# Kernel tuning notes

Hardware: AMD Instinct MI355X
Metric: run time of the kernel (lower is better)

## Reference

```python
import jax, jax.numpy as jnp
import numpy as np

EPS = 1e-13

def masked_softmax(scores, mask):
    # scores: [B, L1, L2], mask: [B, L2] binary float
    # ESIM-style: softmax(scores * mask) * mask, renormalized.
    m = mask[:, None, :]                      # [B, 1, L2]
    r = jax.nn.softmax(scores * m, axis=-1) * m
    return r / (r.sum(axis=-1, keepdims=True) + EPS)

def weighted_sum(attn, tensor, mask):
    # attn: [B, L1, L2], tensor: [B, L2, D], mask: [B, L1]
    return jnp.matmul(attn, tensor) * mask[:, :, None]

def setup_inputs() -> dict:
    key = jax.random.key(0)
    k1, k2, k3, k4 = jax.random.split(key, 4)
    B, Lp, Lh, D = 64, 512, 512, 600
    encoded_premise = jax.random.normal(k1, (B, Lp, D), dtype=jnp.float32)
    encoded_hypothesis = jax.random.normal(k2, (B, Lh, D), dtype=jnp.float32)
    # binary padding masks (1 = valid token)
    premise_mask = (jax.random.uniform(k3, (B, Lp)) > 0.15).astype(jnp.float32)
    hypothesis_mask = (jax.random.uniform(k4, (B, Lh)) > 0.15).astype(jnp.float32)
    return {"encoded_premise": encoded_premise, "premise_mask": premise_mask,
            "encoded_hypothesis": encoded_hypothesis, "hypothesis_mask": hypothesis_mask}

def reference(encoded_premise, premise_mask, encoded_hypothesis, hypothesis_mask):
    # shared cross-attention score matrix [B, Lp, Lh]
    attn = jnp.einsum('bpd,bhd->bph', encoded_premise, encoded_hypothesis)
    a_p = masked_softmax(attn, hypothesis_mask)                    # [B, Lp, Lh]
    a_h = masked_softmax(attn.transpose(0, 2, 1), premise_mask)    # [B, Lh, Lp]
    weighted_premise = weighted_sum(a_p, encoded_hypothesis, premise_mask)      # [B, Lp, D]
    weighted_hypothesis = weighted_sum(a_h, encoded_premise, hypothesis_mask)   # [B, Lh, D]
    return (weighted_premise, weighted_hypothesis)
```

## Files before the change

### kernel.cpp

```cpp
#include <hip/hip_runtime.h>
#include <hip/hip_bf16.h>

#define DEVB 64
#define LSEQ 512
#define DDIM 600
#define KPAD 608

typedef short short8 __attribute__((ext_vector_type(8)));
typedef float f32x4 __attribute__((ext_vector_type(4)));
typedef _Float16 f16x8 __attribute__((ext_vector_type(8)));
typedef _Float16 f16x4 __attribute__((ext_vector_type(4)));

constexpr int LDP = 40;

__device__ __forceinline__ unsigned short f2bf(float x) {
    union { float f; unsigned u; } v; v.f = x;
    unsigned r = v.u + 0x7fffu + ((v.u >> 16) & 1u);
    return (unsigned short)(r >> 16);
}
__device__ __forceinline__ f32x4 mfma16(short8 a, short8 b, f32x4 c) {
    return __builtin_amdgcn_mfma_f32_16x16x32_bf16(a, b, c, 0, 0, 0);
}
__device__ __forceinline__ f32x4 mfma16h(f16x8 a, f16x8 b, f32x4 c) {
    return __builtin_amdgcn_mfma_f32_16x16x32_f16(a, b, c, 0, 0, 0);
}

__global__ __launch_bounds__(256) void prep(
    const float* __restrict__ X, _Float16* __restrict__ Xhi,
    _Float16* __restrict__ Xlo)
{
    int g = blockIdx.x * 256 + threadIdx.x;
    int row  = g / 152;
    int slot = g - row * 152;
    int d = slot << 2;
    f16x4 hi = {0, 0, 0, 0}, lo = {0, 0, 0, 0};
    if (d < DDIM) {
        float4 x = *(const float4*)(X + (size_t)row * DDIM + d);
        hi[0] = (_Float16)x.x; lo[0] = (_Float16)(x.x - (float)hi[0]);
        hi[1] = (_Float16)x.y; lo[1] = (_Float16)(x.y - (float)hi[1]);
        hi[2] = (_Float16)x.z; lo[2] = (_Float16)(x.z - (float)hi[2]);
        hi[3] = (_Float16)x.w; lo[3] = (_Float16)(x.w - (float)hi[3]);
    }
    *(f16x4*)(Xhi + (size_t)row * KPAD + d) = hi;
    if (Xlo) *(f16x4*)(Xlo + (size_t)row * KPAD + d) = lo;
}

__global__ __launch_bounds__(256) void attn_gemm(
    const _Float16* __restrict__ Phi, const _Float16* __restrict__ Plo,
    const _Float16* __restrict__ Hhi, float* __restrict__ attn)
{
    const int bid = blockIdx.x;
    const int swz = (bid & 7) * 128 + (bid >> 3);
    const int b  = swz >> 4;
    const int pt = ((swz >> 2) & 3) << 7;
    const int ht = (swz & 3) << 7;
    const _Float16* Pbh = Phi + (size_t)b * LSEQ * KPAD;
    const _Float16* Pbl = Plo + (size_t)b * LSEQ * KPAD;
    const _Float16* Hb  = Hhi + (size_t)b * LSEQ * KPAD;
    float* Ab = attn + (size_t)b * LSEQ * LSEQ;

    __shared__ _Float16 Ah[128 * LDP], Al[128 * LDP], Bh[128 * LDP];

    const int t    = threadIdx.x;
    const int lane = t & 63;
    const int wave = t >> 6;
    const int wm = (wave >> 1) << 6;
    const int wn = (wave & 1) << 6;
    const int fr = lane & 15;
    const int fq = lane >> 4;

    const int srow = t >> 2;
    const int sc8  = (t & 3) << 3;

    f16x8 pf[6];
    auto issue = [&](int k0) {
#pragma unroll
        for (int r = 0; r < 2; ++r) {
            int row = srow + (r << 6);
            const size_t off = (size_t)row * KPAD + k0 + sc8;
            pf[r * 3 + 0] = *(const f16x8*)(Pbh + (size_t)(pt)*KPAD + off);
            pf[r * 3 + 1] = *(const f16x8*)(Pbl + (size_t)(pt)*KPAD + off);
            pf[r * 3 + 2] = *(const f16x8*)(Hb  + (size_t)(ht)*KPAD + off);
        }
    };
    issue(0);

    f32x4 acc[4][4];
#pragma unroll
    for (int i = 0; i < 4; ++i)
#pragma unroll
        for (int j = 0; j < 4; ++j) acc[i][j] = (f32x4){0.f, 0.f, 0.f, 0.f};

    constexpr int NK = KPAD / 32;
    for (int it = 0; it < NK; ++it) {
#pragma unroll
        for (int r = 0; r < 2; ++r) {
            int row = srow + (r << 6);
            *(f16x8*)&Ah[row * LDP + sc8] = pf[r * 3 + 0];
            *(f16x8*)&Al[row * LDP + sc8] = pf[r * 3 + 1];
            *(f16x8*)&Bh[row * LDP + sc8] = pf[r * 3 + 2];
        }
        __syncthreads();
        if (it + 1 < NK) issue((it + 1) << 5);

        f16x8 ah[4], al[4], bh[4];
#pragma unroll
        for (int i = 0; i < 4; ++i) {
            ah[i] = *(const f16x8*)&Ah[(wm + (i << 4) + fr) * LDP + (fq << 3)];
            al[i] = *(const f16x8*)&Al[(wm + (i << 4) + fr) * LDP + (fq << 3)];
            bh[i] = *(const f16x8*)&Bh[(wn + (i << 4) + fr) * LDP + (fq << 3)];
        }
#pragma unroll
        for (int mi = 0; mi < 4; ++mi)
#pragma unroll
            for (int ni = 0; ni < 4; ++ni) {
                f32x4 c = acc[mi][ni];
                c = mfma16h(ah[mi], bh[ni], c);
                c = mfma16h(al[mi], bh[ni], c);
                acc[mi][ni] = c;
            }
        __syncthreads();
    }

#pragma unroll
    for (int mi = 0; mi < 4; ++mi)
#pragma unroll
        for (int ni = 0; ni < 4; ++ni)
#pragma unroll
            for (int j = 0; j < 4; ++j) {
                int p = pt + wm + (mi << 4) + (fq << 2) + j;
                int h = ht + wn + (ni << 4) + fr;
                Ab[(size_t)p * LSEQ + h] = acc[mi][ni][j];
            }
}

__global__ __launch_bounds__(256) void row_stats_w1(
    const float* __restrict__ attn, const float* __restrict__ hmask,
    float* __restrict__ M1, float* __restrict__ R1,
    unsigned short* __restrict__ W1)
{
    int rowid = (blockIdx.x << 2) + (threadIdx.x >> 6);
    int lane  = threadIdx.x & 63;
    int b     = rowid >> 9;
    const float* row = attn + (size_t)rowid * LSEQ;
    const float* hm  = hmask + (b << 9);

    float4 s0 = *(const float4*)(row + (lane << 3));
    float4 s1 = *(const float4*)(row + (lane << 3) + 4);
    float4 m0 = *(const float4*)(hm + (lane << 3));
    float4 m1 = *(const float4*)(hm + (lane << 3) + 4);

    float v[8], mk[8];
    v[0] = s0.x * m0.x; mk[0] = m0.x;
    v[1] = s0.y * m0.y; mk[1] = m0.y;
    v[2] = s0.z * m0.z; mk[2] = m0.z;
    v[3] = s0.w * m0.w; mk[3] = m0.w;
    v[4] = s1.x * m1.x; mk[4] = m1.x;
    v[5] = s1.y * m1.y; mk[5] = m1.y;
    v[6] = s1.z * m1.z; mk[6] = m1.z;
    v[7] = s1.w * m1.w; mk[7] = m1.w;

    float mx = -1e30f;
#pragma unroll
    for (int i = 0; i < 8; ++i) mx = fmaxf(mx, v[i]);
#pragma unroll
    for (int off = 32; off; off >>= 1) mx = fmaxf(mx, __shfl_xor(mx, off));

    float T = 0.f, S = 0.f;
#pragma unroll
    for (int i = 0; i < 8; ++i) {
        float e = __expf(v[i] - mx);
        S += e;
        T += mk[i] * e;
    }
#pragma unroll
    for (int off = 32; off; off >>= 1) { T += __shfl_xor(T, off); S += __shfl_xor(S, off); }

    float R = 1.f / (T + 1e-13f * S);
    if (lane == 0) { M1[rowid] = mx; R1[rowid] = R; }

    if (W1) {
        union { short8 vv; unsigned short u[8]; } wv;
#pragma unroll
        for (int i = 0; i < 8; ++i)
            wv.u[i] = f2bf(mk[i] * __expf(v[i] - mx) * R);
        *(short8*)(W1 + (size_t)rowid * LSEQ + (lane << 3)) = wv.vv;
    }
}

__global__ __launch_bounds__(256) void col_stats(
    const float* __restrict__ attn, const float* __restrict__ pmask,
    float* __restrict__ M2, float* __restrict__ R2)
{
    int b  = blockIdx.x >> 3;
    int h0 = (blockIdx.x & 7) << 6;
    int lane = threadIdx.x & 63;
    int wave = threadIdx.x >> 6;
    int h = h0 + lane;
    const float* Ab = attn + (size_t)b * LSEQ * LSEQ;
    const float* pm = pmask + (b << 9);

    float mx[4] = {-1e30f, -1e30f, -1e30f, -1e30f};
    float T[4]  = {0.f, 0.f, 0.f, 0.f};
    float S[4]  = {0.f, 0.f, 0.f, 0.f};

    for (int p = wave << 7; p < (wave << 7) + 128; p += 4) {
#pragma unroll
        for (int j = 0; j < 4; ++j) {
            float s = Ab[(size_t)(p + j) * LSEQ + h];
            float m = pm[p + j];
            float v = s * m;
            float nm = fmaxf(mx[j], v);
            float sc = __expf(mx[j] - nm);
            float e  = __expf(v - nm);
            T[j] = T[j] * sc + m * e;
            S[j] = S[j] * sc + e;
            mx[j] = nm;
        }
    }
    float gm = fmaxf(fmaxf(mx[0], mx[1]), fmaxf(mx[2], mx[3]));
    float gT = 0.f, gS = 0.f;
#pragma unroll
    for (int j = 0; j < 4; ++j) {
        float sc = __expf(mx[j] - gm);
        gT += T[j] * sc;
        gS += S[j] * sc;
    }

    __shared__ float sM[4][64], sT[4][64], sS[4][64];
    sM[wave][lane] = gm; sT[wave][lane] = gT; sS[wave][lane] = gS;
    __syncthreads();
    if (wave == 0) {
        float fm = sM[0][lane];
#pragma unroll
        for (int w = 1; w < 4; ++w) fm = fmaxf(fm, sM[w][lane]);
        float fT = 0.f, fS = 0.f;
#pragma unroll
        for (int w = 0; w < 4; ++w) {
            float sc = __expf(sM[w][lane] - fm);
            fT += sT[w][lane] * sc;
            fS += sS[w][lane] * sc;
        }
        M2[(b << 9) + h] = fm;
        R2[(b << 9) + h] = 1.f / (fT + 1e-13f * fS);
    }
}

__global__ __launch_bounds__(256) void w2gen(
    const float* __restrict__ attn, const float* __restrict__ pmask,
    const float* __restrict__ M2, const float* __restrict__ R2,
    unsigned short* __restrict__ W2)
{
    int blk = blockIdx.x;
    int b  = blk >> 5;
    int p0 = ((blk >> 2) & 7) << 6;
    int h0 = (blk & 3) << 7;
    const float* Ab = attn + (size_t)b * LSEQ * LSEQ;
    const float* pm = pmask + (b << 9);

    __shared__ float sM[128], sR[128];
    __shared__ unsigned short T[128 * 66];
    int t = threadIdx.x;
    if (t < 128) { sM[t] = M2[(b << 9) + h0 + t]; sR[t] = R2[(b << 9) + h0 + t]; }
    __syncthreads();

#pragma unroll
    for (int it = 0; it < 8; ++it) {
        int g  = t + (it << 8);
        int pi = g >> 5;
        int hc = (g & 31) << 2;
        float4 x = *(const float4*)(Ab + (size_t)(p0 + pi) * LSEQ + h0 + hc);
        float pv = pm[p0 + pi];
        ushort4 w;
        if (pv != 0.f) {
            w.x = f2bf(__expf(x.x - sM[hc + 0]) * sR[hc + 0]);
            w.y = f2bf(__expf(x.y - sM[hc + 1]) * sR[hc + 1]);
            w.z = f2bf(__expf(x.z - sM[hc + 2]) * sR[hc + 2]);
            w.w = f2bf(__expf(x.w - sM[hc + 3]) * sR[hc + 3]);
        } else { w.x = 0; w.y = 0; w.z = 0; w.w = 0; }
        T[(hc + 0) * 66 + pi] = w.x;
        T[(hc + 1) * 66 + pi] = w.y;
        T[(hc + 2) * 66 + pi] = w.z;
        T[(hc + 3) * 66 + pi] = w.w;
    }
    __syncthreads();

    int h  = t >> 1;
    int po = (t & 1) << 5;
    unsigned buf[16];
#pragma unroll
    for (int i = 0; i < 16; ++i)
        buf[i] = *(const unsigned*)&T[h * 66 + po + 2 * i];
    unsigned* dst = (unsigned*)(W2 + ((size_t)(b << 9) + h0 + h) * LSEQ + p0 + po);
#pragma unroll
    for (int i = 0; i < 4; ++i)
        *(uint4*)(dst + 4 * i) = *(uint4*)&buf[4 * i];
}

__global__ __launch_bounds__(256) void transcvt(
    const float* __restrict__ X, unsigned short* __restrict__ XT)
{
    int blk = blockIdx.x;
    int b   = blk / 80;
    int rem = blk % 80;
    int r0  = (rem / 10) << 6;
    int d0  = (rem % 10) << 6;
    const float* Xb = X + (size_t)b * LSEQ * DDIM;
    unsigned short* Tb = XT + (size_t)b * DDIM * LSEQ;

    __shared__ unsigned short T[64 * 66];
    int t = threadIdx.x;
#pragma unroll
    for (int it = 0; it < 4; ++it) {
        int g  = t + (it << 8);
        int ri = g >> 4;
        int dc = (g & 15) << 2;
        if (d0 + dc < DDIM) {
            float4 x = *(const float4*)(Xb + (size_t)(r0 + ri) * DDIM + d0 + dc);
            T[(dc + 0) * 66 + ri] = f2bf(x.x);
            T[(dc + 1) * 66 + ri] = f2bf(x.y);
            T[(dc + 2) * 66 + ri] = f2bf(x.z);
            T[(dc + 3) * 66 + ri] = f2bf(x.w);
        }
    }
    __syncthreads();

    int d  = t >> 2;
    int ch = (t & 3) << 4;
    if (d0 + d < DDIM) {
        unsigned buf[8];
#pragma unroll
        for (int i = 0; i < 8; ++i)
            buf[i] = *(const unsigned*)&T[d * 66 + ch + 2 * i];
        unsigned* dst = (unsigned*)(Tb + (size_t)(d0 + d) * LSEQ + r0 + ch);
        *(uint4*)(dst)     = *(uint4*)&buf[0];
        *(uint4*)(dst + 4) = *(uint4*)&buf[4];
    }
}

__global__ __launch_bounds__(256) void gemm_bf(
    const unsigned short* __restrict__ W, const unsigned short* __restrict__ BT,
    const float* __restrict__ mask_m, float* __restrict__ out)
{
    const int bid = blockIdx.x;
    const int swz = (bid & 7) * 160 + (bid >> 3);
    const int b   = swz / 20;
    const int rem = swz % 20;
    const int m0  = (rem / 5) << 7;
    const int n0  = (rem % 5) << 7;
    const unsigned short* Wb = W  + (size_t)b * LSEQ * LSEQ;
    const unsigned short* Bb = BT + (size_t)b * DDIM * LSEQ;

    __shared__ unsigned short Wl[128 * LDP];
    __shared__ unsigned short Bl[128 * LDP];
    __shared__ float Mm[128];

    const int t    = threadIdx.x;
    const int lane = t & 63;
    const int wave = t >> 6;
    const int wm = (wave >> 1) << 6;
    const int wn = (wave & 1) << 6;
    const int fr = lane & 15;
    const int fq = lane >> 4;

    if (t < 128) Mm[t] = mask_m[(b << 9) + m0 + t];

    const int srow = t >> 2;
    const int sc8  = (t & 3) << 3;

    short8 pw[2], pb[2];
    auto issue = [&](int k0) {
#pragma unroll
        for (int r = 0; r < 2; ++r) {
            int row = srow + (r << 6);
            pw[r] = *(const short8*)(Wb + (size_t)(m0 + row) * LSEQ + k0 + sc8);
            int nrow = n0 + row;
            short8 bv = {0, 0, 0, 0, 0, 0, 0, 0};
            if (nrow < DDIM) bv = *(const short8*)(Bb + (size_t)nrow * LSEQ + k0 + sc8);
            pb[r] = bv;
        }
    };
    issue(0);

    f32x4 acc[4][4];
#pragma unroll
    for (int i = 0; i < 4; ++i)
#pragma unroll
        for (int j = 0; j < 4; ++j) acc[i][j] = (f32x4){0.f, 0.f, 0.f, 0.f};

    for (int k0 = 0; k0 < LSEQ; k0 += 32) {
#pragma unroll
        for (int r = 0; r < 2; ++r) {
            int row = srow + (r << 6);
            *(short8*)&Wl[row * LDP + sc8] = pw[r];
            *(short8*)&Bl[row * LDP + sc8] = pb[r];
        }
        __syncthreads();
        if (k0 + 32 < LSEQ) issue(k0 + 32);

        short8 af[4], bfr[4];
#pragma unroll
        for (int i = 0; i < 4; ++i) {
            af[i]  = *(const short8*)&Wl[(wm + (i << 4) + fr) * LDP + (fq << 3)];
            bfr[i] = *(const short8*)&Bl[(wn + (i << 4) + fr) * LDP + (fq << 3)];
        }
#pragma unroll
        for (int mi = 0; mi < 4; ++mi)
#pragma unroll
            for (int ni = 0; ni < 4; ++ni)
                acc[mi][ni] = mfma16(af[mi], bfr[ni], acc[mi][ni]);
        __syncthreads();
    }

#pragma unroll
    for (int mi = 0; mi < 4; ++mi)
#pragma unroll
        for (int j = 0; j < 4; ++j) {
            int row = wm + (mi << 4) + (fq << 2) + j;
            float mm = Mm[row];
#pragma unroll
            for (int ni = 0; ni < 4; ++ni) {
                int d = n0 + wn + (ni << 4) + fr;
                if (d < DDIM)
                    out[((size_t)(b << 9) + m0 + row) * DDIM + d] = mm * acc[mi][ni][j];
            }
        }
}

template <int TRANSA>
__global__ __launch_bounds__(256) void wsum(
    const float* __restrict__ attn, const float* __restrict__ Bsrc,
    const float* __restrict__ mask_k, const float* __restrict__ mask_m,
    const float* __restrict__ Mst, const float* __restrict__ Rst,
    float* __restrict__ out)
{
    const int blk = blockIdx.x;
    const int b   = blk / 20;
    const int rem = blk % 20;
    const int m0  = (rem / 5) << 7;
    const int n0  = (rem % 5) << 7;

    const float* Ab  = attn + (size_t)b * LSEQ * LSEQ;
    const float* Bb  = Bsrc + (size_t)b * LSEQ * DDIM;
    const float* mkb = mask_k + (b << 9);

    __shared__ unsigned short Wl[128 * LDP];
    __shared__ unsigned short Bl[128 * LDP];
    __shared__ float Ml[128], Rl[128], Mm[128];

    const int t    = threadIdx.x;
    const int lane = t & 63;
    const int wave = t >> 6;
    const int wm = (wave >> 1) << 6;
    const int wn = (wave & 1) << 6;
    const int fr = lane & 15;
    const int fq = lane >> 4;

    if (t < 128) {
        Ml[t] = Mst[(b << 9) + m0 + t];
        Rl[t] = Rst[(b << 9) + m0 + t];
        Mm[t] = mask_m[(b << 9) + m0 + t];
    }
    __syncthreads();

    f32x4 acc[4][4];
#pragma unroll
    for (int i = 0; i < 4; ++i)
#pragma unroll
        for (int j = 0; j < 4; ++j) acc[i][j] = (f32x4){0.f, 0.f, 0.f, 0.f};

    for (int k0 = 0; k0 < LSEQ; k0 += 32) {
        if constexpr (TRANSA == 0) {
#pragma unroll
            for (int r = 0; r < 4; ++r) {
                int idx = t + (r << 8);
                int row = idx >> 3;
                int c4  = (idx & 7) << 2;
                float4 x  = *(const float4*)(Ab + (size_t)(m0 + row) * LSEQ + k0 + c4);
                float4 km = *(const float4*)(mkb + k0 + c4);
                float Mv = Ml[row], Rv = Rl[row];
                ushort4 w;
                w.x = (km.x != 0.f) ? f2bf(__expf(x.x - Mv) * Rv) : (unsigned short)0;
                w.y = (km.y != 0.f) ? f2bf(__expf(x.y - Mv) * Rv) : (unsigned short)0;
                w.z = (km.z != 0.f) ? f2bf(__expf(x.z - Mv) * Rv) : (unsigned short)0;
                w.w = (km.w != 0.f) ? f2bf(__expf(x.w - Mv) * Rv) : (unsigned short)0;
                *(ushort4*)&Wl[row * LDP + c4] = w;
            }
        } else {
#pragma unroll
            for (int r = 0; r < 4; ++r) {
                int mh = t & 127;
                int pq = (t >> 7) + (r << 1);
                float Mv = Ml[mh], Rv = Rl[mh];
                ushort4 w;
#pragma unroll
                for (int j = 0; j < 4; ++j) {
                    int k = k0 + (pq << 2) + j;
                    float x  = Ab[(size_t)k * LSEQ + m0 + mh];
                    float km = mkb[k];
                    ((unsigned short*)&w)[j] =
                        (km != 0.f) ? f2bf(__expf(x - Mv) * Rv) : (unsigned short)0;
                }
                *(ushort4*)&Wl[mh * LDP + (pq << 2)] = w;
            }
        }
#pragma unroll
        for (int r = 0; r < 4; ++r) {
            int d  = t & 127;
            int kq = (t >> 7) + (r << 1);
            bool valid = (n0 + d) < DDIM;
            ushort4 v;
#pragma unroll
            for (int j = 0; j < 4; ++j) {
                int k = k0 + (kq << 2) + j;
                float x = valid ? Bb[(size_t)k * DDIM + n0 + d] : 0.f;
                ((unsigned short*)&v)[j] = f2bf(x);
            }
            *(ushort4*)&Bl[d * LDP + (kq << 2)] = v;
        }
        __syncthreads();

        short8 af[4], bfr[4];
#pragma unroll
        for (int i = 0; i < 4; ++i) {
            af[i]  = *(const short8*)&Wl[(wm + (i << 4) + fr) * LDP + (fq << 3)];
            bfr[i] = *(const short8*)&Bl[(wn + (i << 4) + fr) * LDP + (fq << 3)];
        }
#pragma unroll
        for (int mi = 0; mi < 4; ++mi)
#pragma unroll
            for (int ni = 0; ni < 4; ++ni)
                acc[mi][ni] = mfma16(af[mi], bfr[ni], acc[mi][ni]);
        __syncthreads();
    }

#pragma unroll
    for (int mi = 0; mi < 4; ++mi)
#pragma unroll
        for (int j = 0; j < 4; ++j) {
            int row = wm + (mi << 4) + (fq << 2) + j;
            float mm = Mm[row];
#pragma unroll
            for (int ni = 0; ni < 4; ++ni) {
                int d = n0 + wn + (ni << 4) + fr;
                if (d < DDIM)
                    out[((size_t)(b << 9) + m0 + row) * DDIM + d] = mm * acc[mi][ni][j];
            }
        }
}

extern "C" void kernel_launch(void* const* d_in, const int* in_sizes, int n_in,
                              void* d_out, int out_size, void* d_ws, size_t ws_size,
                              hipStream_t stream)
{
    const float* P  = (const float*)d_in[0];
    const float* pm = (const float*)d_in[1];
    const float* H  = (const float*)d_in[2];
    const float* hm = (const float*)d_in[3];
    float* out = (float*)d_out;
    char* ws = (char*)d_ws;

    const size_t pk_elems = (size_t)DEVB * LSEQ * KPAD;
    _Float16* Phi = (_Float16*)d_out;
    _Float16* Plo = Phi + pk_elems;
    _Float16* Hhi = Plo + pk_elems;

    const size_t bt_bytes   = (size_t)DEVB * DDIM * LSEQ * 2;
    const size_t w_bytes    = (size_t)DEVB * LSEQ * LSEQ * 2;
    const size_t stat_bytes = (size_t)DEVB * LSEQ * 4;
    const size_t fast_need  = 2 * bt_bytes + 2 * w_bytes + 4 * stat_bytes;

    const int prep_grid = DEVB * LSEQ * 152 / 256;

    if (ws_size >= fast_need) {
        float* attn = (float*)ws;
        unsigned short* hT = (unsigned short*)ws;
        unsigned short* pT = (unsigned short*)(ws + bt_bytes);
        unsigned short* W1 = (unsigned short*)(ws + 2 * bt_bytes);
        unsigned short* W2 = (unsigned short*)(ws + 2 * bt_bytes + w_bytes);
        float* M1 = (float*)(ws + 2 * bt_bytes + 2 * w_bytes);
        float* R1 = M1 + DEVB * LSEQ;
        float* M2 = R1 + DEVB * LSEQ;
        float* R2 = M2 + DEVB * LSEQ;

        prep<<<prep_grid, 256, 0, stream>>>(P, Phi, Plo);
        prep<<<prep_grid, 256, 0, stream>>>(H, Hhi, nullptr);
        attn_gemm<<<DEVB * 16, 256, 0, stream>>>(Phi, Plo, Hhi, attn);
        row_stats_w1<<<DEVB * LSEQ / 4, 256, 0, stream>>>(attn, hm, M1, R1, W1);
        col_stats<<<DEVB * 8, 256, 0, stream>>>(attn, pm, M2, R2);
        w2gen<<<DEVB * 32, 256, 0, stream>>>(attn, pm, M2, R2, W2);
        transcvt<<<DEVB * 80, 256, 0, stream>>>(H, hT);
        transcvt<<<DEVB * 80, 256, 0, stream>>>(P, pT);
        gemm_bf<<<DEVB * 20, 256, 0, stream>>>(W1, hT, pm, out);
        gemm_bf<<<DEVB * 20, 256, 0, stream>>>(W2, pT, hm,
                                               out + (size_t)DEVB * LSEQ * DDIM);
    } else {
        float* attn = (float*)ws;
        float* M1 = (float*)(ws + (size_t)DEVB * LSEQ * LSEQ * 4);
        float* R1 = M1 + DEVB * LSEQ;
        float* M2 = R1 + DEVB * LSEQ;
        float* R2 = M2 + DEVB * LSEQ;

        prep<<<prep_grid, 256, 0, stream>>>(P, Phi, Plo);
        prep<<<prep_grid, 256, 0, stream>>>(H, Hhi, nullptr);
        attn_gemm<<<DEVB * 16, 256, 0, stream>>>(Phi, Plo, Hhi, attn);
        row_stats_w1<<<DEVB * LSEQ / 4, 256, 0, stream>>>(attn, hm, M1, R1, nullptr);
        col_stats<<<DEVB * 8, 256, 0, stream>>>(attn, pm, M2, R2);
        wsum<0><<<DEVB * 20, 256, 0, stream>>>(attn, H, hm, pm, M1, R1, out);
        wsum<1><<<DEVB * 20, 256, 0, stream>>>(attn, P, pm, hm, M2, R2,
                                               out + (size_t)DEVB * LSEQ * DDIM);
    }
}
```

Baseline: 335.2 us.

## Fuse prep with transpose, merge row/col stats, double-buffer GEMMs, switch to fp16

The prep and transpose-convert kernels become one kernel that writes the fp16 hi/lo splits and the transposed fp16 operand together, and the K padding is removed in favour of guarded loads. Row and column softmax statistics are now computed in a single pass over the attention matrix, with a small merge kernel for the column partials. Both GEMM kernels move to double-buffered LDS with one barrier per step, and the weighted-sum GEMM switches from bf16 to fp16 operands. Together these aim to cut global memory passes and kernel launches, at the cost of more LDS, a different rounding behaviour, and workspace laid out partly inside the output buffer.

```diff
diff --git a/kernel.cpp b/kernel.cpp
--- a/kernel.cpp
+++ b/kernel.cpp
@@ -4,7 +4,6 @@
 #define DEVB 64
 #define LSEQ 512
 #define DDIM 600
-#define KPAD 608
 
 typedef short short8 __attribute__((ext_vector_type(8)));
 typedef float f32x4 __attribute__((ext_vector_type(4)));
@@ -25,24 +24,55 @@
     return __builtin_amdgcn_mfma_f32_16x16x32_f16(a, b, c, 0, 0, 0);
 }
 
-__global__ __launch_bounds__(256) void prep(
+__global__ __launch_bounds__(256) void prep_t(
     const float* __restrict__ X, _Float16* __restrict__ Xhi,
-    _Float16* __restrict__ Xlo)
-{
-    int g = blockIdx.x * 256 + threadIdx.x;
-    int row  = g / 152;
-    int slot = g - row * 152;
-    int d = slot << 2;
-    f16x4 hi = {0, 0, 0, 0}, lo = {0, 0, 0, 0};
-    if (d < DDIM) {
-        float4 x = *(const float4*)(X + (size_t)row * DDIM + d);
-        hi[0] = (_Float16)x.x; lo[0] = (_Float16)(x.x - (float)hi[0]);
-        hi[1] = (_Float16)x.y; lo[1] = (_Float16)(x.y - (float)hi[1]);
-        hi[2] = (_Float16)x.z; lo[2] = (_Float16)(x.z - (float)hi[2]);
-        hi[3] = (_Float16)x.w; lo[3] = (_Float16)(x.w - (float)hi[3]);
-    }
-    *(f16x4*)(Xhi + (size_t)row * KPAD + d) = hi;
-    if (Xlo) *(f16x4*)(Xlo + (size_t)row * KPAD + d) = lo;
+    _Float16* __restrict__ Xlo, _Float16* __restrict__ XT)
+{
+    int blk = blockIdx.x;
+    int b   = blk / 80;
+    int rem = blk % 80;
+    int r0  = (rem / 10) << 6;
+    int d0  = (rem % 10) << 6;
+    const float* Xb = X + (size_t)b * LSEQ * DDIM;
+    _Float16* Hib = Xhi + (size_t)b * LSEQ * DDIM;
+    _Float16* Lob = Xlo ? (Xlo + (size_t)b * LSEQ * DDIM) : nullptr;
+
+    __shared__ _Float16 T[64 * 66];
+    int t = threadIdx.x;
+#pragma unroll
+    for (int it = 0; it < 4; ++it) {
+        int g  = t + (it << 8);
+        int ri = g >> 4;
+        int dc = (g & 15) << 2;
+        if (d0 + dc < DDIM) {
+            float4 x = *(const float4*)(Xb + (size_t)(r0 + ri) * DDIM + d0 + dc);
+            f16x4 hi, lo;
+            hi[0] = (_Float16)x.x; lo[0] = (_Float16)(x.x - (float)hi[0]);
+            hi[1] = (_Float16)x.y; lo[1] = (_Float16)(x.y - (float)hi[1]);
+            hi[2] = (_Float16)x.z; lo[2] = (_Float16)(x.z - (float)hi[2]);
+            hi[3] = (_Float16)x.w; lo[3] = (_Float16)(x.w - (float)hi[3]);
+            *(f16x4*)(Hib + (size_t)(r0 + ri) * DDIM + d0 + dc) = hi;
+            if (Lob) *(f16x4*)(Lob + (size_t)(r0 + ri) * DDIM + d0 + dc) = lo;
+            T[(dc + 0) * 66 + ri] = hi[0];
+            T[(dc + 1) * 66 + ri] = hi[1];
+            T[(dc + 2) * 66 + ri] = hi[2];
+            T[(dc + 3) * 66 + ri] = hi[3];
+        }
+    }
+    if (XT) {
+        __syncthreads();
+        int d  = t >> 2;
+        int ch = (t & 3) << 4;
+        if (d0 + d < DDIM) {
+            unsigned buf[8];
+#pragma unroll
+            for (int i = 0; i < 8; ++i)
+                buf[i] = *(const unsigned*)&T[d * 66 + ch + 2 * i];
+            unsigned* dst = (unsigned*)(XT + ((size_t)b * DDIM + d0 + d) * LSEQ + r0 + ch);
+            *(uint4*)(dst)     = *(uint4*)&buf[0];
+            *(uint4*)(dst + 4) = *(uint4*)&buf[4];
+        }
+    }
 }
 
 __global__ __launch_bounds__(256) void attn_gemm(
@@ -54,12 +84,12 @@
     const int b  = swz >> 4;
     const int pt = ((swz >> 2) & 3) << 7;
     const int ht = (swz & 3) << 7;
-    const _Float16* Pbh = Phi + (size_t)b * LSEQ * KPAD;
-    const _Float16* Pbl = Plo + (size_t)b * LSEQ * KPAD;
-    const _Float16* Hb  = Hhi + (size_t)b * LSEQ * KPAD;
+    const _Float16* Pbh = Phi + ((size_t)b * LSEQ + pt) * DDIM;
+    const _Float16* Pbl = Plo + ((size_t)b * LSEQ + pt) * DDIM;
+    const _Float16* Hb  = Hhi + ((size_t)b * LSEQ + ht) * DDIM;
     float* Ab = attn + (size_t)b * LSEQ * LSEQ;
 
-    __shared__ _Float16 Ah[128 * LDP], Al[128 * LDP], Bh[128 * LDP];
+    __shared__ _Float16 Ah[2][128 * LDP], Al[2][128 * LDP], Bh[2][128 * LDP];
 
     const int t    = threadIdx.x;
     const int lane = t & 63;
@@ -68,22 +98,35 @@
     const int wn = (wave & 1) << 6;
     const int fr = lane & 15;
     const int fq = lane >> 4;
-
     const int srow = t >> 2;
     const int sc8  = (t & 3) << 3;
 
     f16x8 pf[6];
+    const f16x8 zz = {0, 0, 0, 0, 0, 0, 0, 0};
     auto issue = [&](int k0) {
+        bool ok = (k0 + sc8) < DDIM;
+#pragma unroll
+        for (int r = 0; r < 2; ++r) {
+            size_t off = (size_t)(srow + (r << 6)) * DDIM + k0 + sc8;
+            pf[r * 3 + 0] = ok ? *(const f16x8*)(Pbh + off) : zz;
+            pf[r * 3 + 1] = ok ? *(const f16x8*)(Pbl + off) : zz;
+            pf[r * 3 + 2] = ok ? *(const f16x8*)(Hb  + off) : zz;
+        }
+    };
+    auto wr = [&](int buf) {
 #pragma unroll
         for (int r = 0; r < 2; ++r) {
             int row = srow + (r << 6);
-            const size_t off = (size_t)row * KPAD + k0 + sc8;
-            pf[r * 3 + 0] = *(const f16x8*)(Pbh + (size_t)(pt)*KPAD + off);
-            pf[r * 3 + 1] = *(const f16x8*)(Pbl + (size_t)(pt)*KPAD + off);
-            pf[r * 3 + 2] = *(const f16x8*)(Hb  + (size_t)(ht)*KPAD + off);
+            *(f16x8*)&Ah[buf][row * LDP + sc8] = pf[r * 3 + 0];
+            *(f16x8*)&Al[buf][row * LDP + sc8] = pf[r * 3 + 1];
+            *(f16x8*)&Bh[buf][row * LDP + sc8] = pf[r * 3 + 2];
         }
     };
+
     issue(0);
+    wr(0);
+    issue(32);
+    __syncthreads();
 
     f32x4 acc[4][4];
 #pragma unroll
@@ -91,24 +134,19 @@
 #pragma unroll
         for (int j = 0; j < 4; ++j) acc[i][j] = (f32x4){0.f, 0.f, 0.f, 0.f};
 
-    constexpr int NK = KPAD / 32;
+    constexpr int NK = 19;
+    int cur = 0;
     for (int it = 0; it < NK; ++it) {
-#pragma unroll
-        for (int r = 0; r < 2; ++r) {
-            int row = srow + (r << 6);
-            *(f16x8*)&Ah[row * LDP + sc8] = pf[r * 3 + 0];
-            *(f16x8*)&Al[row * LDP + sc8] = pf[r * 3 + 1];
-            *(f16x8*)&Bh[row * LDP + sc8] = pf[r * 3 + 2];
-        }
-        __syncthreads();
-        if (it + 1 < NK) issue((it + 1) << 5);
-
         f16x8 ah[4], al[4], bh[4];
 #pragma unroll
         for (int i = 0; i < 4; ++i) {
-            ah[i] = *(const f16x8*)&Ah[(wm + (i << 4) + fr) * LDP + (fq << 3)];
-            al[i] = *(const f16x8*)&Al[(wm + (i << 4) + fr) * LDP + (fq << 3)];
-            bh[i] = *(const f16x8*)&Bh[(wn + (i << 4) + fr) * LDP + (fq << 3)];
+            ah[i] = *(const f16x8*)&Ah[cur][(wm + (i << 4) + fr) * LDP + (fq << 3)];
+            al[i] = *(const f16x8*)&Al[cur][(wm + (i << 4) + fr) * LDP + (fq << 3)];
+            bh[i] = *(const f16x8*)&Bh[cur][(wn + (i << 4) + fr) * LDP + (fq << 3)];
+        }
+        if (it + 1 < NK) {
+            wr(cur ^ 1);
+            if (it + 2 < NK) issue((it + 2) << 5);
         }
 #pragma unroll
         for (int mi = 0; mi < 4; ++mi)
@@ -120,6 +158,7 @@
                 acc[mi][ni] = c;
             }
         __syncthreads();
+        cur ^= 1;
     }
 
 #pragma unroll
@@ -134,122 +173,120 @@
             }
 }
 
-__global__ __launch_bounds__(256) void row_stats_w1(
+__global__ __launch_bounds__(256) void stats_w1(
     const float* __restrict__ attn, const float* __restrict__ hmask,
+    const float* __restrict__ pmask,
     float* __restrict__ M1, float* __restrict__ R1,
-    unsigned short* __restrict__ W1)
-{
-    int rowid = (blockIdx.x << 2) + (threadIdx.x >> 6);
-    int lane  = threadIdx.x & 63;
-    int b     = rowid >> 9;
-    const float* row = attn + (size_t)rowid * LSEQ;
-    const float* hm  = hmask + (b << 9);
-
-    float4 s0 = *(const float4*)(row + (lane << 3));
-    float4 s1 = *(const float4*)(row + (lane << 3) + 4);
+    _Float16* __restrict__ W1,
+    float* __restrict__ Mp, float* __restrict__ Tp, float* __restrict__ Sp)
+{
+    int b      = blockIdx.x >> 3;
+    int stripe = blockIdx.x & 7;
+    int lane   = threadIdx.x & 63;
+    int wave   = threadIdx.x >> 6;
+    const float* hm = hmask + (b << 9);
+    const float* pm = pmask + (b << 9);
+
     float4 m0 = *(const float4*)(hm + (lane << 3));
     float4 m1 = *(const float4*)(hm + (lane << 3) + 4);
-
-    float v[8], mk[8];
-    v[0] = s0.x * m0.x; mk[0] = m0.x;
-    v[1] = s0.y * m0.y; mk[1] = m0.y;
-    v[2] = s0.z * m0.z; mk[2] = m0.z;
-    v[3] = s0.w * m0.w; mk[3] = m0.w;
-    v[4] = s1.x * m1.x; mk[4] = m1.x;
-    v[5] = s1.y * m1.y; mk[5] = m1.y;
-    v[6] = s1.z * m1.z; mk[6] = m1.z;
-    v[7] = s1.w * m1.w; mk[7] = m1.w;
-
-    float mx = -1e30f;
-#pragma unroll
-    for (int i = 0; i < 8; ++i) mx = fmaxf(mx, v[i]);
-#pragma unroll
-    for (int off = 32; off; off >>= 1) mx = fmaxf(mx, __shfl_xor(mx, off));
-
-    float T = 0.f, S = 0.f;
-#pragma unroll
-    for (int i = 0; i < 8; ++i) {
-        float e = __expf(v[i] - mx);
-        S += e;
-        T += mk[i] * e;
-    }
-#pragma unroll
-    for (int off = 32; off; off >>= 1) { T += __shfl_xor(T, off); S += __shfl_xor(S, off); }
-
-    float R = 1.f / (T + 1e-13f * S);
-    if (lane == 0) { M1[rowid] = mx; R1[rowid] = R; }
-
-    if (W1) {
-        union { short8 vv; unsigned short u[8]; } wv;
-#pragma unroll
-        for (int i = 0; i < 8; ++i)
-            wv.u[i] = f2bf(mk[i] * __expf(v[i] - mx) * R);
-        *(short8*)(W1 + (size_t)rowid * LSEQ + (lane << 3)) = wv.vv;
-    }
-}
-
-__global__ __launch_bounds__(256) void col_stats(
-    const float* __restrict__ attn, const float* __restrict__ pmask,
-    float* __restrict__ M2, float* __restrict__ R2)
-{
-    int b  = blockIdx.x >> 3;
-    int h0 = (blockIdx.x & 7) << 6;
-    int lane = threadIdx.x & 63;
-    int wave = threadIdx.x >> 6;
-    int h = h0 + lane;
-    const float* Ab = attn + (size_t)b * LSEQ * LSEQ;
-    const float* pm = pmask + (b << 9);
-
-    float mx[4] = {-1e30f, -1e30f, -1e30f, -1e30f};
-    float T[4]  = {0.f, 0.f, 0.f, 0.f};
-    float S[4]  = {0.f, 0.f, 0.f, 0.f};
-
-    for (int p = wave << 7; p < (wave << 7) + 128; p += 4) {
-#pragma unroll
-        for (int j = 0; j < 4; ++j) {
-            float s = Ab[(size_t)(p + j) * LSEQ + h];
-            float m = pm[p + j];
-            float v = s * m;
-            float nm = fmaxf(mx[j], v);
-            float sc = __expf(mx[j] - nm);
-            float e  = __expf(v - nm);
-            T[j] = T[j] * sc + m * e;
-            S[j] = S[j] * sc + e;
-            mx[j] = nm;
-        }
-    }
-    float gm = fmaxf(fmaxf(mx[0], mx[1]), fmaxf(mx[2], mx[3]));
-    float gT = 0.f, gS = 0.f;
-#pragma unroll
-    for (int j = 0; j < 4; ++j) {
-        float sc = __expf(mx[j] - gm);
-        gT += T[j] * sc;
-        gS += S[j] * sc;
-    }
-
-    __shared__ float sM[4][64], sT[4][64], sS[4][64];
-    sM[wave][lane] = gm; sT[wave][lane] = gT; sS[wave][lane] = gS;
+    float mk[8] = {m0.x, m0.y, m0.z, m0.w, m1.x, m1.y, m1.z, m1.w};
+
+    float cM[8], cT[8], cS[8];
+#pragma unroll
+    for (int j = 0; j < 8; ++j) { cM[j] = -1e30f; cT[j] = 0.f; cS[j] = 0.f; }
+
+    for (int i = 0; i < 16; ++i) {
+        int row   = (stripe << 6) + (wave << 4) + i;
+        int rowid = (b << 9) + row;
+        const float* rp = attn + (size_t)rowid * LSEQ + (lane << 3);
+        float4 s0 = *(const float4*)rp;
+        float4 s1 = *(const float4*)(rp + 4);
+        float s[8] = {s0.x, s0.y, s0.z, s0.w, s1.x, s1.y, s1.z, s1.w};
+
+        float v[8];
+#pragma unroll
+        for (int j = 0; j < 8; ++j) v[j] = s[j] * mk[j];
+        float mx = -1e30f;
+#pragma unroll
+        for (int j = 0; j < 8; ++j) mx = fmaxf(mx, v[j]);
+#pragma unroll
+        for (int off = 32; off; off >>= 1) mx = fmaxf(mx, __shfl_xor(mx, off));
+
+        float e[8], T = 0.f, S = 0.f;
+#pragma unroll
+        for (int j = 0; j < 8; ++j) { e[j] = __expf(v[j] - mx); T += mk[j] * e[j]; S += e[j]; }
+#pragma unroll
+        for (int off = 32; off; off >>= 1) { T += __shfl_xor(T, off); S += __shfl_xor(S, off); }
+        float R = 1.f / (T + 1e-13f * S);
+
+        if (W1) {
+            union { f16x8 v8; _Float16 h[8]; } wv;
+#pragma unroll
+            for (int j = 0; j < 8; ++j) wv.h[j] = (_Float16)(mk[j] * e[j] * R);
+            *(f16x8*)(W1 + (size_t)rowid * LSEQ + (lane << 3)) = wv.v8;
+        }
+        if (lane == 0) { M1[rowid] = mx; R1[rowid] = R; }
+
+        float pmv = pm[row];
+#pragma unroll
+        for (int j = 0; j < 8; ++j) {
+            float v2 = s[j] * pmv;
+            float nm = fmaxf(cM[j], v2);
+            float sc = __expf(cM[j] - nm);
+            float e2 = __expf(v2 - nm);
+            cT[j] = cT[j] * sc + pmv * e2;
+            cS[j] = cS[j] * sc + e2;
+            cM[j] = nm;
+        }
+    }
+
+    __shared__ float LM[4][512], LT[4][512], LS[4][512];
+#pragma unroll
+    for (int j = 0; j < 8; ++j) {
+        int c = (lane << 3) + j;
+        LM[wave][c] = cM[j]; LT[wave][c] = cT[j]; LS[wave][c] = cS[j];
+    }
     __syncthreads();
-    if (wave == 0) {
-        float fm = sM[0][lane];
-#pragma unroll
-        for (int w = 1; w < 4; ++w) fm = fmaxf(fm, sM[w][lane]);
-        float fT = 0.f, fS = 0.f;
+
+    size_t base = (size_t)((b << 3) + stripe) * 512;
+    for (int cc = threadIdx.x; cc < 512; cc += 256) {
+        float gm = fmaxf(fmaxf(LM[0][cc], LM[1][cc]), fmaxf(LM[2][cc], LM[3][cc]));
+        float gT = 0.f, gS = 0.f;
 #pragma unroll
         for (int w = 0; w < 4; ++w) {
-            float sc = __expf(sM[w][lane] - fm);
-            fT += sT[w][lane] * sc;
-            fS += sS[w][lane] * sc;
-        }
-        M2[(b << 9) + h] = fm;
-        R2[(b << 9) + h] = 1.f / (fT + 1e-13f * fS);
-    }
+            float sc = __expf(LM[w][cc] - gm);
+            gT += LT[w][cc] * sc;
+            gS += LS[w][cc] * sc;
+        }
+        Mp[base + cc] = gm; Tp[base + cc] = gT; Sp[base + cc] = gS;
+    }
+}
+
+__global__ __launch_bounds__(256) void col_merge(
+    const float* __restrict__ Mp, const float* __restrict__ Tp,
+    const float* __restrict__ Sp, float* __restrict__ M2, float* __restrict__ R2)
+{
+    int b = blockIdx.x >> 1;
+    int c = ((blockIdx.x & 1) << 8) + threadIdx.x;
+    float gm = -1e30f, gT = 0.f, gS = 0.f;
+#pragma unroll
+    for (int st = 0; st < 8; ++st) {
+        size_t idx = (size_t)((b << 3) + st) * 512 + c;
+        float m = Mp[idx], tt = Tp[idx], ss = Sp[idx];
+        float nm  = fmaxf(gm, m);
+        float sc1 = __expf(gm - nm), sc2 = __expf(m - nm);
+        gT = gT * sc1 + tt * sc2;
+        gS = gS * sc1 + ss * sc2;
+        gm = nm;
+    }
+    M2[(b << 9) + c] = gm;
+    R2[(b << 9) + c] = 1.f / (gT + 1e-13f * gS);
 }
 
 __global__ __launch_bounds__(256) void w2gen(
     const float* __restrict__ attn, const float* __restrict__ pmask,
     const float* __restrict__ M2, const float* __restrict__ R2,
-    unsigned short* __restrict__ W2)
+    _Float16* __restrict__ W2)
 {
     int blk = blockIdx.x;
     int b  = blk >> 5;
@@ -259,7 +296,7 @@
     const float* pm = pmask + (b << 9);
 
     __shared__ float sM[128], sR[128];
-    __shared__ unsigned short T[128 * 66];
+    __shared__ _Float16 T[128 * 66];
     int t = threadIdx.x;
     if (t < 128) { sM[t] = M2[(b << 9) + h0 + t]; sR[t] = R2[(b << 9) + h0 + t]; }
     __syncthreads();
@@ -271,17 +308,17 @@
         int hc = (g & 31) << 2;
         float4 x = *(const float4*)(Ab + (size_t)(p0 + pi) * LSEQ + h0 + hc);
         float pv = pm[p0 + pi];
-        ushort4 w;
+        _Float16 w0 = 0, w1 = 0, w2 = 0, w3 = 0;
         if (pv != 0.f) {
-            w.x = f2bf(__expf(x.x - sM[hc + 0]) * sR[hc + 0]);
-            w.y = f2bf(__expf(x.y - sM[hc + 1]) * sR[hc + 1]);
-            w.z = f2bf(__expf(x.z - sM[hc + 2]) * sR[hc + 2]);
-            w.w = f2bf(__expf(x.w - sM[hc + 3]) * sR[hc + 3]);
-        } else { w.x = 0; w.y = 0; w.z = 0; w.w = 0; }
-        T[(hc + 0) * 66 + pi] = w.x;
-        T[(hc + 1) * 66 + pi] = w.y;
-        T[(hc + 2) * 66 + pi] = w.z;
-        T[(hc + 3) * 66 + pi] = w.w;
+            w0 = (_Float16)(__expf(x.x - sM[hc + 0]) * sR[hc + 0]);
+            w1 = (_Float16)(__expf(x.y - sM[hc + 1]) * sR[hc + 1]);
+            w2 = (_Float16)(__expf(x.z - sM[hc + 2]) * sR[hc + 2]);
+            w3 = (_Float16)(__expf(x.w - sM[hc + 3]) * sR[hc + 3]);
+        }
+        T[(hc + 0) * 66 + pi] = w0;
+        T[(hc + 1) * 66 + pi] = w1;
+        T[(hc + 2) * 66 + pi] = w2;
+        T[(hc + 3) * 66 + pi] = w3;
     }
     __syncthreads();
 
@@ -297,49 +334,8 @@
         *(uint4*)(dst + 4 * i) = *(uint4*)&buf[4 * i];
 }
 
-__global__ __launch_bounds__(256) void transcvt(
-    const float* __restrict__ X, unsigned short* __restrict__ XT)
-{
-    int blk = blockIdx.x;
-    int b   = blk / 80;
-    int rem = blk % 80;
-    int r0  = (rem / 10) << 6;
-    int d0  = (rem % 10) << 6;
-    const float* Xb = X + (size_t)b * LSEQ * DDIM;
-    unsigned short* Tb = XT + (size_t)b * DDIM * LSEQ;
-
-    __shared__ unsigned short T[64 * 66];
-    int t = threadIdx.x;
-#pragma unroll
-    for (int it = 0; it < 4; ++it) {
-        int g  = t + (it << 8);
-        int ri = g >> 4;
-        int dc = (g & 15) << 2;
-        if (d0 + dc < DDIM) {
-            float4 x = *(const float4*)(Xb + (size_t)(r0 + ri) * DDIM + d0 + dc);
-            T[(dc + 0) * 66 + ri] = f2bf(x.x);
-            T[(dc + 1) * 66 + ri] = f2bf(x.y);
-            T[(dc + 2) * 66 + ri] = f2bf(x.z);
-            T[(dc + 3) * 66 + ri] = f2bf(x.w);
-        }
-    }
-    __syncthreads();
-
-    int d  = t >> 2;
-    int ch = (t & 3) << 4;
-    if (d0 + d < DDIM) {
-        unsigned buf[8];
-#pragma unroll
-        for (int i = 0; i < 8; ++i)
-            buf[i] = *(const unsigned*)&T[d * 66 + ch + 2 * i];
-        unsigned* dst = (unsigned*)(Tb + (size_t)(d0 + d) * LSEQ + r0 + ch);
-        *(uint4*)(dst)     = *(uint4*)&buf[0];
-        *(uint4*)(dst + 4) = *(uint4*)&buf[4];
-    }
-}
-
-__global__ __launch_bounds__(256) void gemm_bf(
-    const unsigned short* __restrict__ W, const unsigned short* __restrict__ BT,
+__global__ __launch_bounds__(256) void gemm_fp16(
+    const _Float16* __restrict__ W, const _Float16* __restrict__ BT,
     const float* __restrict__ mask_m, float* __restrict__ out)
 {
     const int bid = blockIdx.x;
@@ -348,11 +344,11 @@
     const int rem = swz % 20;
     const int m0  = (rem / 5) << 7;
     const int n0  = (rem % 5) << 7;
-    const unsigned short* Wb = W  + (size_t)b * LSEQ * LSEQ;
-    const unsigned short* Bb = BT + (size_t)b * DDIM * LSEQ;
-
-    __shared__ unsigned short Wl[128 * LDP];
-    __shared__ unsigned short Bl[128 * LDP];
+    const _Float16* Wb = W  + (size_t)b * LSEQ * LSEQ;
+    const _Float16* Bb = BT + (size_t)b * DDIM * LSEQ;
+
+    __shared__ _Float16 Wl[2][128 * LDP];
+    __shared__ _Float16 Bl[2][128 * LDP];
     __shared__ float Mm[128];
 
     const int t    = threadIdx.x;
@@ -362,54 +358,62 @@
     const int wn = (wave & 1) << 6;
     const int fr = lane & 15;
     const int fq = lane >> 4;
-
-    if (t < 128) Mm[t] = mask_m[(b << 9) + m0 + t];
-
     const int srow = t >> 2;
     const int sc8  = (t & 3) << 3;
 
-    short8 pw[2], pb[2];
+    if (t < 128) Mm[t] = mask_m[(b << 9) + m0 + t];
+
+    f16x8 pw[2], pb[2];
+    const f16x8 zz = {0, 0, 0, 0, 0, 0, 0, 0};
     auto issue = [&](int k0) {
 #pragma unroll
         for (int r = 0; r < 2; ++r) {
             int row = srow + (r << 6);
-            pw[r] = *(const short8*)(Wb + (size_t)(m0 + row) * LSEQ + k0 + sc8);
+            pw[r] = *(const f16x8*)(Wb + (size_t)(m0 + row) * LSEQ + k0 + sc8);
             int nrow = n0 + row;
-            short8 bv = {0, 0, 0, 0, 0, 0, 0, 0};
-            if (nrow < DDIM) bv = *(const short8*)(Bb + (size_t)nrow * LSEQ + k0 + sc8);
-            pb[r] = bv;
+            pb[r] = (nrow < DDIM) ? *(const f16x8*)(Bb + (size_t)nrow * LSEQ + k0 + sc8) : zz;
         }
     };
-    issue(0);
-
-    f32x4 acc[4][4];
-#pragma unroll
-    for (int i = 0; i < 4; ++i)
-#pragma unroll
-        for (int j = 0; j < 4; ++j) acc[i][j] = (f32x4){0.f, 0.f, 0.f, 0.f};
-
-    for (int k0 = 0; k0 < LSEQ; k0 += 32) {
+    auto wr = [&](int buf) {
 #pragma unroll
         for (int r = 0; r < 2; ++r) {
             int row = srow + (r << 6);
-            *(short8*)&Wl[row * LDP + sc8] = pw[r];
-            *(short8*)&Bl[row * LDP + sc8] = pb[r];
-        }
+            *(f16x8*)&Wl[buf][row * LDP + sc8] = pw[r];
+            *(f16x8*)&Bl[buf][row * LDP + sc8] = pb[r];
+        }
+    };
+
+    issue(0);
+    wr(0);
+    issue(32);
+    __syncthreads();
+
+    f32x4 acc[4][4];
+#pragma unroll
+    for (int i = 0; i < 4; ++i)
+#pragma unroll
+        for (int j = 0; j < 4; ++j) acc[i][j] = (f32x4){0.f, 0.f, 0.f, 0.f};
+
+    constexpr int NK = 16;
+    int cur = 0;
+    for (int it = 0; it < NK; ++it) {
+        f16x8 af[4], bfr[4];
+#pragma unroll
+        for (int i = 0; i < 4; ++i) {
+            af[i]  = *(const f16x8*)&Wl[cur][(wm + (i << 4) + fr) * LDP + (fq << 3)];
+            bfr[i] = *(const f16x8*)&Bl[cur][(wn + (i << 4) + fr) * LDP + (fq << 3)];
+        }
+        if (it + 1 < NK) {
+            wr(cur ^ 1);
+            if (it + 2 < NK) issue((it + 2) << 5);
+        }
+#pragma unroll
+        for (int mi = 0; mi < 4; ++mi)
+#pragma unroll
+            for (int ni = 0; ni < 4; ++ni)
+                acc[mi][ni] = mfma16h(af[mi], bfr[ni], acc[mi][ni]);
         __syncthreads();
-        if (k0 + 32 < LSEQ) issue(k0 + 32);
-
-        short8 af[4], bfr[4];
-#pragma unroll
-        for (int i = 0; i < 4; ++i) {
-            af[i]  = *(const short8*)&Wl[(wm + (i << 4) + fr) * LDP + (fq << 3)];
-            bfr[i] = *(const short8*)&Bl[(wn + (i << 4) + fr) * LDP + (fq << 3)];
-        }
-#pragma unroll
-        for (int mi = 0; mi < 4; ++mi)
-#pragma unroll
-            for (int ni = 0; ni < 4; ++ni)
-                acc[mi][ni] = mfma16(af[mi], bfr[ni], acc[mi][ni]);
-        __syncthreads();
+        cur ^= 1;
     }
 
 #pragma unroll
@@ -558,56 +562,55 @@
     const float* H  = (const float*)d_in[2];
     const float* hm = (const float*)d_in[3];
     float* out = (float*)d_out;
+    char* o  = (char*)d_out;
     char* ws = (char*)d_ws;
 
-    const size_t pk_elems = (size_t)DEVB * LSEQ * KPAD;
-    _Float16* Phi = (_Float16*)d_out;
-    _Float16* Plo = Phi + pk_elems;
-    _Float16* Hhi = Plo + pk_elems;
-
-    const size_t bt_bytes   = (size_t)DEVB * DDIM * LSEQ * 2;
-    const size_t w_bytes    = (size_t)DEVB * LSEQ * LSEQ * 2;
-    const size_t stat_bytes = (size_t)DEVB * LSEQ * 4;
-    const size_t fast_need  = 2 * bt_bytes + 2 * w_bytes + 4 * stat_bytes;
-
-    const int prep_grid = DEVB * LSEQ * 152 / 256;
+    const size_t E = (size_t)DEVB * LSEQ * DDIM;
+
+    _Float16* Phi = (_Float16*)o;
+    _Float16* Plo = Phi + E;
+    _Float16* Hhi = Plo + E;
+    _Float16* hT  = Hhi + E;
+    _Float16* W1  = Hhi;
+
+    const size_t fast_need = 143654912;
 
     if (ws_size >= fast_need) {
-        float* attn = (float*)ws;
-        unsigned short* hT = (unsigned short*)ws;
-        unsigned short* pT = (unsigned short*)(ws + bt_bytes);
-        unsigned short* W1 = (unsigned short*)(ws + 2 * bt_bytes);
-        unsigned short* W2 = (unsigned short*)(ws + 2 * bt_bytes + w_bytes);
-        float* M1 = (float*)(ws + 2 * bt_bytes + 2 * w_bytes);
-        float* R1 = M1 + DEVB * LSEQ;
-        float* M2 = R1 + DEVB * LSEQ;
-        float* R2 = M2 + DEVB * LSEQ;
-
-        prep<<<prep_grid, 256, 0, stream>>>(P, Phi, Plo);
-        prep<<<prep_grid, 256, 0, stream>>>(H, Hhi, nullptr);
+        float*     attn = (float*)ws;
+        _Float16*  pT   = (_Float16*)(ws + 67108864);
+        _Float16*  W2   = (_Float16*)(ws + 67108864 + 39321600);
+        float*     Mp   = (float*)(ws + 139984896);
+        float*     Tp   = Mp + (size_t)DEVB * 8 * 512;
+        float*     Sp   = Tp + (size_t)DEVB * 8 * 512;
+        float*     M1   = Sp + (size_t)DEVB * 8 * 512;
+        float*     R1   = M1 + DEVB * LSEQ;
+        float*     M2   = R1 + DEVB * LSEQ;
+        float*     R2   = M2 + DEVB * LSEQ;
+
+        prep_t<<<DEVB * 80, 256, 0, stream>>>(P, Phi, Plo, pT);
+        prep_t<<<DEVB * 80, 256, 0, stream>>>(H, Hhi, nullptr, hT);
         attn_gemm<<<DEVB * 16, 256, 0, stream>>>(Phi, Plo, Hhi, attn);
-        row_stats_w1<<<DEVB * LSEQ / 4, 256, 0, stream>>>(attn, hm, M1, R1, W1);
-        col_stats<<<DEVB * 8, 256, 0, stream>>>(attn, pm, M2, R2);
+        stats_w1<<<DEVB * 8, 256, 0, stream>>>(attn, hm, pm, M1, R1, W1, Mp, Tp, Sp);
+        col_merge<<<DEVB * 2, 256, 0, stream>>>(Mp, Tp, Sp, M2, R2);
         w2gen<<<DEVB * 32, 256, 0, stream>>>(attn, pm, M2, R2, W2);
-        transcvt<<<DEVB * 80, 256, 0, stream>>>(H, hT);
-        transcvt<<<DEVB * 80, 256, 0, stream>>>(P, pT);
-        gemm_bf<<<DEVB * 20, 256, 0, stream>>>(W1, hT, pm, out);
-        gemm_bf<<<DEVB * 20, 256, 0, stream>>>(W2, pT, hm,
-                                               out + (size_t)DEVB * LSEQ * DDIM);
+        gemm_fp16<<<DEVB * 20, 256, 0, stream>>>(W1, hT, pm, out);
+        gemm_fp16<<<DEVB * 20, 256, 0, stream>>>(W2, pT, hm, out + E);
     } else {
         float* attn = (float*)ws;
-        float* M1 = (float*)(ws + (size_t)DEVB * LSEQ * LSEQ * 4);
-        float* R1 = M1 + DEVB * LSEQ;
-        float* M2 = R1 + DEVB * LSEQ;
-        float* R2 = M2 + DEVB * LSEQ;
-
-        prep<<<prep_grid, 256, 0, stream>>>(P, Phi, Plo);
-        prep<<<prep_grid, 256, 0, stream>>>(H, Hhi, nullptr);
+        float* Mp   = (float*)(ws + 67108864);
+        float* Tp   = Mp + (size_t)DEVB * 8 * 512;
+        float* Sp   = Tp + (size_t)DEVB * 8 * 512;
+        float* M1   = Sp + (size_t)DEVB * 8 * 512;
+        float* R1   = M1 + DEVB * LSEQ;
+        float* M2   = R1 + DEVB * LSEQ;
+        float* R2   = M2 + DEVB * LSEQ;
+
+        prep_t<<<DEVB * 80, 256, 0, stream>>>(P, Phi, Plo, nullptr);
+        prep_t<<<DEVB * 80, 256, 0, stream>>>(H, Hhi, nullptr, nullptr);
         attn_gemm<<<DEVB * 16, 256, 0, stream>>>(Phi, Plo, Hhi, attn);
-        row_stats_w1<<<DEVB * LSEQ / 4, 256, 0, stream>>>(attn, hm, M1, R1, nullptr);
-        col_stats<<<DEVB * 8, 256, 0, stream>>>(attn, pm, M2, R2);
+        stats_w1<<<DEVB * 8, 256, 0, stream>>>(attn, hm, pm, M1, R1, nullptr, Mp, Tp, Sp);
+        col_merge<<<DEVB * 2, 256, 0, stream>>>(Mp, Tp, Sp, M2, R2);
         wsum<0><<<DEVB * 20, 256, 0, stream>>>(attn, H, hm, pm, M1, R1, out);
-        wsum<1><<<DEVB * 20, 256, 0, stream>>>(attn, P, pm, hm, M2, R2,
-                                               out + (size_t)DEVB * LSEQ * DDIM);
-    }
-}
+        wsum<1><<<DEVB * 20, 256, 0, stream>>>(attn, P, pm, hm, M2, R2, out + E);
+    }
+}
```

Result: faster. 327.1 us (-2.4%).
